# Performance work log

Measured on AMD Instinct MI355X. Metric: run time of the kernel, lower is better.

The kernel has to match this reference:

```python
import jax, jax.numpy as jnp
import numpy as np

NL, NS, NE = 16, 256, 100   # nlatent, nspatial, n_embd
B, P, T = 2, 2, 12


def _xavier(key, shape):
    # torch xavier_uniform: fan_in = shape[1]*prod(rest), fan_out = shape[0]*prod(rest)
    rf = int(np.prod(shape[2:])) if len(shape) > 2 else 1
    fan_in, fan_out = shape[1] * rf, shape[0] * rf
    b = float(np.sqrt(6.0 / (fan_in + fan_out)))
    return jax.random.uniform(key, shape, jnp.float32, -b, b)


def setup_inputs() -> dict:
    key = jax.random.key(0)
    ks = jax.random.split(key, 8)
    x = jax.random.normal(ks[0], (B, P, T, NL, NS), jnp.float32)
    K = _xavier(ks[1], (NS, NS, NL))
    Q = _xavier(ks[2], (NS, NS, NL))
    V = _xavier(ks[3], (NS, NS, NL))
    Aoo = jnp.ones((NS, NS), jnp.float32)
    # Ann is initialized to zeros in the module; use nonzero values so the
    # clamped geometric recurrence over time is actually exercised.
    Ann = jax.random.uniform(ks[4], (NE,), jnp.float32, -0.9, 0.9)
    Aon = _xavier(ks[5], (NS, NS, NE))
    Ano = _xavier(ks[6], (NS, NS, NE))
    w = jnp.ones((NS,), jnp.float32) / NS
    return {"x": x, "K": K, "Q": Q, "V": V, "Aoo": Aoo,
            "Ann": Ann, "Aon": Aon, "Ano": Ano, "w": w}


def reference(x, K, Q, V, Aoo, Ann, Aon, Ano, w):
    # kvt[B,p,T,X,Y] = sum_{x,c} Q[Y,x,c] K[X,x,c] x[B,p,T,c,x]
    kvt = jnp.einsum('Yxc,Xxc,BpTcx->BpTXY', Q, K, x)
    Aon_c = jnp.clip(Aon, -1.0, 1.0)
    Ano_c = jnp.clip(Ano, -1.0, 1.0)

    # t = T-1 term (elementwise Aoo) and t = T-2 term
    h = Aoo[None, None, None] * kvt[:, :, -1:]
    h = h + jnp.einsum('xyn,XYn,BpTXY->BpTxy', Aon_c, Ano_c, kvt[:, :, -2:-1])

    nT = x.shape[2]
    # Ann sequence used in the loop: A_2 = Ann (raw), A_{j+1} = clip(A_j * Ann)
    def step(a, _):
        return jnp.clip(a * Ann, -1.0, 1.0), a
    _, A_seq = jax.lax.scan(step, Ann, None, length=nT - 2)  # [T-2, n], A_seq[j-2]=A_j

    # loop index j=2..T-1 touches time slice t = T-1-j, i.e. t = T-3 .. 0
    s = jnp.einsum('XYn,BpJXY->BpJn', Ano_c, kvt[:, :, :nT - 2])  # J = t in 0..T-3
    A_t = A_seq[::-1]                       # align A_j with time index t = T-1-j
    s2 = jnp.einsum('Jn,BpJn->Bpn', A_t, s)
    h = h + jnp.einsum('xyn,Bpn->Bpxy', Aon_c, s2)[:, :, None]  # [B,p,1,x,y]

    q = jnp.einsum('Xxc,Bpcx->BpcX', V, x[:, :, -1])
    y = jnp.einsum('x,BpcX,BpTXx->BpTc', w, q, h)  # [B,p,1,c]
    return y
```

## Files before the change

kernel.cpp:

```cpp
#include <hip/hip_runtime.h>
#include <hip/hip_fp16.h>


using f32x4 = __attribute__((ext_vector_type(4))) float;
using half8 = __attribute__((ext_vector_type(8))) _Float16;
using half4 = __attribute__((ext_vector_type(4))) _Float16;

#define KVT_STRIDE 3145728ull
#define KS 4

__device__ inline float clip1(float v) { return fminf(fmaxf(v, -1.f), 1.f); }

__device__ inline half8 mul8(uint4 a, uint4 b) {
    half8 x = __builtin_bit_cast(half8, a);
    half8 y = __builtin_bit_cast(half8, b);
    return x * y;
}

__device__ __forceinline__ void gl_lds16(const void* g, void* l) {
    __builtin_amdgcn_global_load_lds(
        (const __attribute__((address_space(1))) void*)g,
        (__attribute__((address_space(3))) void*)l, 16, 0, 0);
}

__global__ void prep_kernel(const float* __restrict__ K, const float* __restrict__ Q,
                            const float* __restrict__ xin,
                            __half* __restrict__ Kh, __half* __restrict__ Qh,
                            __half* __restrict__ u_t)
{
    int b = blockIdx.x, t = threadIdx.x;
    if (b < 512) {
        bool isK = (b < 256);
        int bb = isK ? b : b - 256;
        size_t base = (size_t)bb * 4096 + t * 16;
        const f32x4* src = (const f32x4*)((isK ? K : Q) + base);
        __half* dst = (isK ? Kh : Qh) + base;
        #pragma unroll
        for (int j = 0; j < 2; ++j) {
            f32x4 v0 = src[j * 2], v1 = src[j * 2 + 1];
            half8 h;
            h[0] = (_Float16)v0.x; h[1] = (_Float16)v0.y;
            h[2] = (_Float16)v0.z; h[3] = (_Float16)v0.w;
            h[4] = (_Float16)v1.x; h[5] = (_Float16)v1.y;
            h[6] = (_Float16)v1.z; h[7] = (_Float16)v1.w;
            *(half8*)(dst + j * 8) = h;
        }
    } else {
        int bt = b - 512;
        const float* src = xin + (size_t)bt * 4096;
        int xx = t;
        half8 lo, hi;
        #pragma unroll
        for (int c = 0; c < 8; ++c)  lo[c] = (_Float16)src[c * 256 + xx];
        #pragma unroll
        for (int c = 0; c < 8; ++c)  hi[c] = (_Float16)src[(c + 8) * 256 + xx];
        half8* dst = (half8*)(u_t + (size_t)bt * 4096 + xx * 16);
        dst[0] = lo; dst[1] = hi;
    }
}

__global__ __launch_bounds__(256, 3) void gemm_kvt(
    const __half* __restrict__ Kh, const __half* __restrict__ Qh,
    const __half* __restrict__ u_t, __half* __restrict__ kvtp)
{
    __shared__ __half As[128][64];
    __shared__ __half Bs[2][128][64];
    __shared__ __half u_s[1024];

    int bid = blockIdx.x;
    int work = (bid & 7) * 96 + (bid >> 3);
    int kc = work / 192;
    int rem = work - kc * 192;
    int tile = rem / 48;
    int bt = rem - tile * 48;
    int Xb = (tile >> 1) * 128, Yb = (tile & 1) * 128;
    int kbase = kc * 1024;

    int tid = threadIdx.x;
    if (tid < 128)
        *(uint4*)&u_s[tid * 8] = *(const uint4*)(u_t + (size_t)bt * 4096 + kbase + tid * 8);
    __syncthreads();

    int wave = tid >> 6, lane = tid & 63;

    int arow = tid >> 1;
    int ap0 = (tid & 1) * 4;
    const __half* gA = Kh + (size_t)(Xb + arow) * 4096 + kbase + ap0 * 8;
    int arsw = arow & 7;

    int brow = wave * 32 + (lane >> 3);
    int bq = (lane & 7) ^ ((lane >> 3) & 7);
    const __half* gB = Qh + (size_t)(Yb + brow) * 4096 + kbase + bq * 8;

    int wr = (wave >> 1) * 64, wc = (wave & 1) * 64;
    int lrow = lane & 15, kg = lane >> 4;
    int fb0 = ((0 * 4 + kg) ^ (lrow & 7)) << 4;
    int fb1 = ((1 * 4 + kg) ^ (lrow & 7)) << 4;

    f32x4 acc[4][4];
    f32x4 zero = {0.f, 0.f, 0.f, 0.f};
    #pragma unroll
    for (int m = 0; m < 4; ++m)
        #pragma unroll
        for (int n = 0; n < 4; ++n) acc[m][n] = zero;

    #define LOAD_A(s, rg)                                                      \
        do {                                                                   \
            const __half* a_ = gA + (s) * 64;                                  \
            _Pragma("unroll")                                                  \
            for (int j_ = 0; j_ < 4; ++j_)                                     \
                rg[j_] = *(const uint4*)(a_ + j_ * 8);                         \
        } while (0)

    #define ISSUE_B(s, buf)                                                    \
        do {                                                                   \
            _Pragma("unroll")                                                  \
            for (int i_ = 0; i_ < 4; ++i_)                                     \
                gl_lds16(gB + (size_t)(i_ * 8) * 4096 + (s) * 64,              \
                         &Bs[buf][wave * 32 + i_ * 8][0]);                     \
        } while (0)

    #define WRITE_A(s, rg)                                                     \
        do {                                                                   \
            _Pragma("unroll")                                                  \
            for (int j_ = 0; j_ < 4; ++j_) {                                   \
                int p_ = ap0 + j_;                                             \
                uint4 uv_ = *(const uint4*)&u_s[(s) * 64 + p_ * 8];            \
                *(half8*)((char*)&As[arow][0] + ((p_ ^ arsw) << 4)) =          \
                    mul8(rg[j_], uv_);                                         \
            }                                                                  \
        } while (0)

    #define COMPUTE(cur)                                                       \
        do {                                                                   \
            _Pragma("unroll")                                                  \
            for (int kh = 0; kh < 2; ++kh) {                                   \
                int fbk = kh ? fb1 : fb0;                                      \
                half8 af[4], bf[4];                                            \
                _Pragma("unroll")                                              \
                for (int m = 0; m < 4; ++m)                                    \
                    af[m] = *(const half8*)((const char*)&As[wr + m * 16 + lrow][0] + fbk); \
                _Pragma("unroll")                                              \
                for (int n = 0; n < 4; ++n)                                    \
                    bf[n] = *(const half8*)((const char*)&Bs[cur][wc + n * 16 + lrow][0] + fbk); \
                _Pragma("unroll")                                              \
                for (int m = 0; m < 4; ++m)                                    \
                    _Pragma("unroll")                                          \
                    for (int n = 0; n < 4; ++n)                                \
                        acc[m][n] = __builtin_amdgcn_mfma_f32_16x16x32_f16(af[m], bf[n], acc[m][n], 0, 0, 0); \
            }                                                                  \
        } while (0)

    #define STEP(s, cset, iset, cur)                                           \
        do {                                                                   \
            if ((s) < 15) asm volatile("s_waitcnt vmcnt(8) lgkmcnt(0)" ::: "memory"); \
            else          asm volatile("s_waitcnt vmcnt(0) lgkmcnt(0)" ::: "memory"); \
            __builtin_amdgcn_s_barrier();                                      \
            __builtin_amdgcn_sched_barrier(0);                                 \
            COMPUTE(cur);                                                      \
            asm volatile("s_waitcnt lgkmcnt(0)" ::: "memory");                 \
            __builtin_amdgcn_s_barrier();                                      \
            __builtin_amdgcn_sched_barrier(0);                                 \
            if ((s) + 2 < 16) {                                                \
                LOAD_A((s) + 2, iset);                                         \
                ISSUE_B((s) + 2, cur);                                         \
            }                                                                  \
            if ((s) + 1 < 16) WRITE_A((s) + 1, cset);                          \
        } while (0)

    uint4 aP[4], aC[4];
    LOAD_A(0, aP);
    ISSUE_B(0, 0);
    LOAD_A(1, aC);
    ISSUE_B(1, 1);
    WRITE_A(0, aP);

    #pragma unroll
    for (int s = 0; s < 16; s += 2) {
        STEP(s,     aC, aP, 0);
        STEP(s + 1, aP, aC, 1);
    }
    #undef STEP
    #undef COMPUTE
    #undef WRITE_A
    #undef ISSUE_B
    #undef LOAD_A

    __half* outp = kvtp + (size_t)kc * KVT_STRIDE + (size_t)bt * 65536;
    int row0 = Xb + wr + kg * 4;
    int col0 = Yb + wc + lrow;
    #pragma unroll
    for (int m = 0; m < 4; ++m)
        #pragma unroll
        for (int n = 0; n < 4; ++n)
            #pragma unroll
            for (int rr = 0; rr < 4; ++rr)
                outp[(size_t)(row0 + m * 16 + rr) * 256 + col0 + n * 16] =
                    __float2half(acc[m][n][rr]);
}

__global__ __launch_bounds__(256) void mid_kernel(
    const float* __restrict__ Ano, const __half* __restrict__ kvtp,
    const float* __restrict__ V, const float* __restrict__ xin,
    const float* __restrict__ Aon, const float* __restrict__ wv,
    float* __restrict__ Sp, float* __restrict__ R, float* __restrict__ W2p)
{
    __shared__ __align__(16) char smem[49792];
    int b = blockIdx.x, tid = threadIdx.x;

    if (b < 256) {
        __half* anoA = (__half*)smem;
        __half* anoB = (__half*)(smem + 12928);
        float (*kvtA)[68] = (float(*)[68])(smem + 25856);
        float (*kvtB)[68] = (float(*)[68])(smem + 37824);
        int k0 = b * 256;

        int lane = tid & 63;
        int bp = tid >> 6;
        bool has2 = lane < 36;
        float acc0[11], acc1[11];
        #pragma unroll
        for (int J = 0; J < 11; ++J) { acc0[J] = 0.f; acc1[J] = 0.f; }

        f32x4 ar[7];
        half8 kr[2][4];

        #define LOAD_SP(cc)                                                    \
            do {                                                               \
                int k0s = k0 + (cc) * 64;                                      \
                const f32x4* asrc = (const f32x4*)(Ano + (size_t)k0s * 100);   \
                _Pragma("unroll")                                              \
                for (int it = 0; it < 7; ++it) {                               \
                    int i = tid + it * 256;                                    \
                    if (i < 1600) ar[it] = __builtin_nontemporal_load(asrc + i); \
                }                                                              \
                _Pragma("unroll")                                              \
                for (int it = 0; it < 2; ++it) {                               \
                    int idx = tid + it * 256;                                  \
                    if (idx < 352) {                                           \
                        int rI = idx >> 3, g = idx & 7;                        \
                        int bpr = rI / 11, Jr = rI - bpr * 11;                 \
                        const __half* p = kvtp + (size_t)(bpr * 12 + Jr) * 65536 + k0s + g * 8; \
                        kr[it][0] = *(const half8*)(p);                        \
                        kr[it][1] = *(const half8*)(p + KVT_STRIDE);           \
                        kr[it][2] = *(const half8*)(p + 2 * KVT_STRIDE);       \
                        kr[it][3] = *(const half8*)(p + 3 * KVT_STRIDE);       \
                    }                                                          \
                }                                                              \
            } while (0)

        #define WRITE_SP(anoDst, kvtDst)                                       \
            do {                                                               \
                _Pragma("unroll")                                              \
                for (int it = 0; it < 7; ++it) {                               \
                    int i = tid + it * 256;                                    \
                    if (i < 1600) {                                            \
                        half4 h;                                               \
                        h[0] = (_Float16)clip1(ar[it].x);                      \
                        h[1] = (_Float16)clip1(ar[it].y);                      \
                        h[2] = (_Float16)clip1(ar[it].z);                      \
                        h[3] = (_Float16)clip1(ar[it].w);                      \
                        *(half4*)&anoDst[i * 4] = h;                           \
                    }                                                          \
                }                                                              \
                _Pragma("unroll")                                              \
                for (int it = 0; it < 2; ++it) {                               \
                    int idx = tid + it * 256;                                  \
                    if (idx < 352) {                                           \
                        int rI = idx >> 3, g = idx & 7;                        \
                        f32x4 lo, hi;                                          \
                        _Pragma("unroll")                                      \
                        for (int j = 0; j < 4; ++j) {                          \
                            lo[j] = (float)kr[it][0][j] + (float)kr[it][1][j]  \
                                  + (float)kr[it][2][j] + (float)kr[it][3][j]; \
                            hi[j] = (float)kr[it][0][j+4] + (float)kr[it][1][j+4] \
                                  + (float)kr[it][2][j+4] + (float)kr[it][3][j+4]; \
                        }                                                      \
                        *(f32x4*)&kvtDst[rI][g * 8]     = lo;                  \
                        *(f32x4*)&kvtDst[rI][g * 8 + 4] = hi;                  \
                    }                                                          \
                }                                                              \
            } while (0)

        #define COMPUTE_SP(anoSrc, kvtSrc)                                     \
            do {                                                               \
                for (int k = 0; k < 64; k += 4) {                              \
                    f32x4 kv[11];                                              \
                    _Pragma("unroll")                                          \
                    for (int J = 0; J < 11; ++J)                               \
                        kv[J] = *(const f32x4*)&kvtSrc[bp * 11 + J][k];        \
                    _Pragma("unroll")                                          \
                    for (int kk = 0; kk < 4; ++kk) {                           \
                        float a0 = (float)anoSrc[(k + kk) * 100 + lane];       \
                        float a1r = (float)anoSrc[(k + kk) * 100 + 64 + lane]; \
                        float a1 = has2 ? a1r : 0.f;                           \
                        _Pragma("unroll")                                      \
                        for (int J = 0; J < 11; ++J) {                         \
                            acc0[J] += kv[J][kk] * a0;                         \
                            acc1[J] += kv[J][kk] * a1;                         \
                        }                                                      \
                    }                                                          \
                }                                                              \
            } while (0)

        LOAD_SP(0);
        WRITE_SP(anoA, kvtA);
        __syncthreads();
        LOAD_SP(1);
        COMPUTE_SP(anoA, kvtA);
        WRITE_SP(anoB, kvtB);
        __syncthreads();
        LOAD_SP(2);
        COMPUTE_SP(anoB, kvtB);
        WRITE_SP(anoA, kvtA);
        __syncthreads();
        LOAD_SP(3);
        COMPUTE_SP(anoA, kvtA);
        WRITE_SP(anoB, kvtB);
        __syncthreads();
        COMPUTE_SP(anoB, kvtB);

        #undef LOAD_SP
        #undef WRITE_SP
        #undef COMPUTE_SP

        float* outb = Sp + ((size_t)b * 4 + bp) * 1100;
        #pragma unroll
        for (int J = 0; J < 11; ++J) {
            outb[J * 100 + lane] = acc0[J];
            if (has2) outb[J * 100 + 64 + lane] = acc1[J];
        }
    } else if (b < 512) {
        float* vrow = (float*)smem;
        int X = b - 256;
        {
            const float4* src = (const float4*)(V + (size_t)X * 4096);
            float4* dst = (float4*)vrow;
            for (int i = tid; i < 1024; i += 256) dst[i] = src[i];
        }
        __syncthreads();
        int bp = tid >> 6, c = (tid >> 2) & 15, g = tid & 3;
        const float* xl = xin + ((size_t)(bp * 12) + 11) * 4096 + c * 256;
        float p0 = 0.f, p1 = 0.f;
        #pragma unroll 2
        for (int x = g * 64; x < g * 64 + 64; x += 2) {
            p0 += xl[x]     * vrow[x * 16 + c];
            p1 += xl[x + 1] * vrow[(x + 1) * 16 + c];
        }
        float p = p0 + p1;
        p += __shfl_xor(p, 1);
        p += __shfl_xor(p, 2);
        if (g == 0) R[((size_t)bp * 256 + X) * 16 + c] = p;
    } else {
        int idx = b - 512;
        int X = idx >> 1, h = idx & 1;
        int g = h * 2 + (tid >> 7), n = tid & 127;
        if (n < 100) {
            const float* base = Aon + (size_t)X * 25600 + (size_t)g * 6400 + n;
            const float* wb = wv + g * 64;
            float a0 = 0.f, a1 = 0.f, a2 = 0.f, a3 = 0.f;
            for (int bb = 0; bb < 64; bb += 4) {
                float v0 = __builtin_nontemporal_load(base + (size_t)(bb + 0) * 100);
                float v1 = __builtin_nontemporal_load(base + (size_t)(bb + 1) * 100);
                float v2 = __builtin_nontemporal_load(base + (size_t)(bb + 2) * 100);
                float v3 = __builtin_nontemporal_load(base + (size_t)(bb + 3) * 100);
                a0 += wb[bb + 0] * clip1(v0);
                a1 += wb[bb + 1] * clip1(v1);
                a2 += wb[bb + 2] * clip1(v2);
                a3 += wb[bb + 3] * clip1(v3);
            }
            W2p[((size_t)g * 256 + X) * 100 + n] = (a0 + a1) + (a2 + a3);
        }
    }
}

__global__ void reduce_s(const float* __restrict__ Sp, float* __restrict__ Sq,
                         float* __restrict__ out)
{
    int bid = blockIdx.x;
    int t = threadIdx.x;
    if (bid == 0 && t < 64) out[t] = 0.f;
    int qq = bid & 7, idx = bid >> 3;
    int bp = idx / 11, J = idx - bp * 11;
    if (t >= 100) return;
    float a0 = 0.f, a1 = 0.f, a2 = 0.f, a3 = 0.f;
    int c0 = qq * 32;
    for (int c = c0; c < c0 + 32; c += 4) {
        a0 += Sp[((size_t)(c + 0) * 4 + bp) * 1100 + J * 100 + t];
        a1 += Sp[((size_t)(c + 1) * 4 + bp) * 1100 + J * 100 + t];
        a2 += Sp[((size_t)(c + 2) * 4 + bp) * 1100 + J * 100 + t];
        a3 += Sp[((size_t)(c + 3) * 4 + bp) * 1100 + J * 100 + t];
    }
    Sq[(size_t)(qq * 44 + idx) * 100 + t] = (a0 + a1) + (a2 + a3);
}

__global__ __launch_bounds__(256) void hw_kernel(const float* __restrict__ Aoo,
                                                 const float* __restrict__ wv,
                                                 const __half* __restrict__ kvtp,
                                                 const float* __restrict__ W2p,
                                                 const float* __restrict__ Sq,
                                                 const float* __restrict__ Ann,
                                                 const float* __restrict__ R,
                                                 float* __restrict__ out)
{
    __shared__ float yp[4][16];
    __shared__ float c2s[128];
    int bp = blockIdx.x >> 6, Xg = blockIdx.x & 63;
    int tid = threadIdx.x;

    if (tid < 128) {
        int n = tid;
        float r = 0.f;
        if (n < 100) {
            float S[11];
            #pragma unroll
            for (int J = 0; J < 11; ++J) {
                float s = 0.f;
                #pragma unroll
                for (int qq = 0; qq < 8; ++qq)
                    s += Sq[(size_t)(qq * 44 + bp * 11 + J) * 100 + n];
                S[J] = s;
            }
            float a = Ann[n];
            float seq[10];
            float v = a;
            seq[0] = v;
            #pragma unroll
            for (int s2 = 1; s2 < 10; ++s2) { v = clip1(v * a); seq[s2] = v; }
            r = S[10];
            #pragma unroll
            for (int J = 0; J < 10; ++J)
                r += seq[9 - J] * S[J];
        }
        c2s[n] = r;
    }
    __syncthreads();

    int wave = tid >> 6, lane = tid & 63;
    int X = Xg * 4 + wave;
    size_t base = (size_t)(bp * 12 + 11) * 65536 + (size_t)X * 256;
    const float* ao = Aoo + (size_t)X * 256;
    float red = 0.f;
    #pragma unroll
    for (int qq = 0; qq < 4; ++qq) {
        int xx = qq * 64 + lane;
        float kvv = 0.f;
        #pragma unroll
        for (int c = 0; c < KS; ++c)
            kvv += __half2float(kvtp[(size_t)c * KVT_STRIDE + base + xx]);
        red += wv[xx] * ao[xx] * kvv;
    }
    float w2a = 0.f, w2b = 0.f;
    #pragma unroll
    for (int g = 0; g < 4; ++g) {
        w2a += W2p[((size_t)g * 256 + X) * 100 + lane];
        if (lane < 36) w2b += W2p[((size_t)g * 256 + X) * 100 + 64 + lane];
    }
    red += c2s[lane] * w2a;
    if (lane < 36)
        red += c2s[64 + lane] * w2b;
    #pragma unroll
    for (int off = 32; off; off >>= 1) red += __shfl_xor(red, off);
    if (lane < 16) yp[wave][lane] = red * R[((size_t)bp * 256 + X) * 16 + lane];
    __syncthreads();
    if (tid < 16) {
        float s = yp[0][tid] + yp[1][tid] + yp[2][tid] + yp[3][tid];
        atomicAdd(&out[bp * 16 + tid], s);
    }
}

extern "C" void kernel_launch(void* const* d_in, const int* in_sizes, int n_in,
                              void* d_out, int out_size, void* d_ws, size_t ws_size,
                              hipStream_t stream)
{
    const float* x   = (const float*)d_in[0];
    const float* K   = (const float*)d_in[1];
    const float* Q   = (const float*)d_in[2];
    const float* V   = (const float*)d_in[3];
    const float* Aoo = (const float*)d_in[4];
    const float* Ann = (const float*)d_in[5];
    const float* Aon = (const float*)d_in[6];
    const float* Ano = (const float*)d_in[7];
    const float* wv  = (const float*)d_in[8];
    float* out = (float*)d_out;

    char* ws = (char*)d_ws;
    const size_t o_Qh   = 0;
    const size_t o_Kh   = o_Qh + (size_t)2 * 1024 * 1024;
    const size_t o_ut   = o_Kh + (size_t)2 * 1024 * 1024;
    const size_t o_kvtp = o_ut + (size_t)512 * 1024;
    const size_t o_Sp   = o_kvtp + (size_t)KS * KVT_STRIDE * 2;
    const size_t o_Sq   = o_Sp + (size_t)256 * 4400 * 4;
    const size_t o_W2   = o_Sq + (size_t)35200 * 4 + 64;
    const size_t o_R    = o_W2 + (size_t)102400 * 4;

    __half* Qh  = (__half*)(ws + o_Qh);
    __half* Kh  = (__half*)(ws + o_Kh);
    __half* u_t = (__half*)(ws + o_ut);
    __half* kvtp = (__half*)(ws + o_kvtp);
    float* Sp   = (float*)(ws + o_Sp);
    float* Sq   = (float*)(ws + o_Sq);
    float* W2p  = (float*)(ws + o_W2);
    float* R    = (float*)(ws + o_R);

    hipLaunchKernelGGL(prep_kernel, dim3(560),  dim3(256), 0, stream,
                       K, Q, x, Kh, Qh, u_t);
    hipLaunchKernelGGL(gemm_kvt,    dim3(768),  dim3(256), 0, stream,
                       Kh, Qh, u_t, kvtp);
    hipLaunchKernelGGL(mid_kernel,  dim3(1024), dim3(256), 0, stream,
                       Ano, kvtp, V, x, Aon, wv, Sp, R, W2p);
    hipLaunchKernelGGL(reduce_s,    dim3(352),  dim3(128), 0, stream, Sp, Sq, out);
    hipLaunchKernelGGL(hw_kernel,   dim3(256),  dim3(256), 0, stream,
                       Aoo, wv, kvtp, W2p, Sq, Ann, R, out);
}
```

Before: 88.09 us.

## Replace reduce_s kernel with atomic accumulation in mid_kernel; vectorize hw loads

Each mid_kernel block now adds its partial S sums straight into the eight-way Sq buffer with float atomics, instead of writing per-block partials that a separate reduce_s kernel summed. Sq and out are zeroed by extra blocks added to prep_kernel. This removes one kernel launch and the round trip of the partial buffer through memory. In exchange it adds atomic contention (32 blocks per address) and a float summation order that varies from run to run. hw_kernel also switches to half4 and float4 vector loads for the kvt, w and Aoo reads.

```diff
diff --git a/kernel.cpp b/kernel.cpp
--- a/kernel.cpp
+++ b/kernel.cpp
@@ -26,7 +26,8 @@
 __global__ void prep_kernel(const float* __restrict__ K, const float* __restrict__ Q,
                             const float* __restrict__ xin,
                             __half* __restrict__ Kh, __half* __restrict__ Qh,
-                            __half* __restrict__ u_t)
+                            __half* __restrict__ u_t,
+                            float* __restrict__ Sq, float* __restrict__ out)
 {
     int b = blockIdx.x, t = threadIdx.x;
     if (b < 512) {
@@ -45,7 +46,7 @@
             h[6] = (_Float16)v1.z; h[7] = (_Float16)v1.w;
             *(half8*)(dst + j * 8) = h;
         }
-    } else {
+    } else if (b < 560) {
         int bt = b - 512;
         const float* src = xin + (size_t)bt * 4096;
         int xx = t;
@@ -56,6 +57,13 @@
         for (int c = 0; c < 8; ++c)  hi[c] = (_Float16)src[(c + 8) * 256 + xx];
         half8* dst = (half8*)(u_t + (size_t)bt * 4096 + xx * 16);
         dst[0] = lo; dst[1] = hi;
+    } else {
+        int zb = b - 560;
+        int i = zb * 1024 + t * 4;
+        f32x4 z = {0.f, 0.f, 0.f, 0.f};
+        if (i + 3 < 35200) *(f32x4*)(Sq + i) = z;
+        else for (int j = 0; j < 4; ++j) if (i + j < 35200) Sq[i + j] = 0.f;
+        if (zb == 0 && t < 64) out[t] = 0.f;
     }
 }
 
@@ -203,7 +211,7 @@
     const float* __restrict__ Ano, const __half* __restrict__ kvtp,
     const float* __restrict__ V, const float* __restrict__ xin,
     const float* __restrict__ Aon, const float* __restrict__ wv,
-    float* __restrict__ Sp, float* __restrict__ R, float* __restrict__ W2p)
+    float* __restrict__ Sq, float* __restrict__ R, float* __restrict__ W2p)
 {
     __shared__ __align__(16) char smem[49792];
     int b = blockIdx.x, tid = threadIdx.x;
@@ -324,11 +332,12 @@
         #undef WRITE_SP
         #undef COMPUTE_SP
 
-        float* outb = Sp + ((size_t)b * 4 + bp) * 1100;
+        int qq = b >> 5;
+        float* sqb = Sq + (size_t)(qq * 44 + bp * 11) * 100;
         #pragma unroll
         for (int J = 0; J < 11; ++J) {
-            outb[J * 100 + lane] = acc0[J];
-            if (has2) outb[J * 100 + 64 + lane] = acc1[J];
+            atomicAdd(&sqb[J * 100 + lane], acc0[J]);
+            if (has2) atomicAdd(&sqb[J * 100 + 64 + lane], acc1[J]);
         }
     } else if (b < 512) {
         float* vrow = (float*)smem;
@@ -374,26 +383,6 @@
     }
 }
 
-__global__ void reduce_s(const float* __restrict__ Sp, float* __restrict__ Sq,
-                         float* __restrict__ out)
-{
-    int bid = blockIdx.x;
-    int t = threadIdx.x;
-    if (bid == 0 && t < 64) out[t] = 0.f;
-    int qq = bid & 7, idx = bid >> 3;
-    int bp = idx / 11, J = idx - bp * 11;
-    if (t >= 100) return;
-    float a0 = 0.f, a1 = 0.f, a2 = 0.f, a3 = 0.f;
-    int c0 = qq * 32;
-    for (int c = c0; c < c0 + 32; c += 4) {
-        a0 += Sp[((size_t)(c + 0) * 4 + bp) * 1100 + J * 100 + t];
-        a1 += Sp[((size_t)(c + 1) * 4 + bp) * 1100 + J * 100 + t];
-        a2 += Sp[((size_t)(c + 2) * 4 + bp) * 1100 + J * 100 + t];
-        a3 += Sp[((size_t)(c + 3) * 4 + bp) * 1100 + J * 100 + t];
-    }
-    Sq[(size_t)(qq * 44 + idx) * 100 + t] = (a0 + a1) + (a2 + a3);
-}
-
 __global__ __launch_bounds__(256) void hw_kernel(const float* __restrict__ Aoo,
                                                  const float* __restrict__ wv,
                                                  const __half* __restrict__ kvtp,
@@ -438,17 +427,20 @@
 
     int wave = tid >> 6, lane = tid & 63;
     int X = Xg * 4 + wave;
-    size_t base = (size_t)(bp * 12 + 11) * 65536 + (size_t)X * 256;
-    const float* ao = Aoo + (size_t)X * 256;
+    size_t base = (size_t)(bp * 12 + 11) * 65536 + (size_t)X * 256 + lane * 4;
     float red = 0.f;
-    #pragma unroll
-    for (int qq = 0; qq < 4; ++qq) {
-        int xx = qq * 64 + lane;
-        float kvv = 0.f;
-        #pragma unroll
-        for (int c = 0; c < KS; ++c)
-            kvv += __half2float(kvtp[(size_t)c * KVT_STRIDE + base + xx]);
-        red += wv[xx] * ao[xx] * kvv;
+    {
+        f32x4 kvs = {0.f, 0.f, 0.f, 0.f};
+        #pragma unroll
+        for (int c = 0; c < KS; ++c) {
+            half4 v = *(const half4*)(kvtp + (size_t)c * KVT_STRIDE + base);
+            #pragma unroll
+            for (int i = 0; i < 4; ++i) kvs[i] += (float)v[i];
+        }
+        f32x4 w4  = *(const f32x4*)(wv + lane * 4);
+        f32x4 ao4 = *(const f32x4*)(Aoo + (size_t)X * 256 + lane * 4);
+        #pragma unroll
+        for (int i = 0; i < 4; ++i) red += w4[i] * ao4[i] * kvs[i];
     }
     float w2a = 0.f, w2b = 0.f;
     #pragma unroll
@@ -489,8 +481,7 @@
     const size_t o_Kh   = o_Qh + (size_t)2 * 1024 * 1024;
     const size_t o_ut   = o_Kh + (size_t)2 * 1024 * 1024;
     const size_t o_kvtp = o_ut + (size_t)512 * 1024;
-    const size_t o_Sp   = o_kvtp + (size_t)KS * KVT_STRIDE * 2;
-    const size_t o_Sq   = o_Sp + (size_t)256 * 4400 * 4;
+    const size_t o_Sq   = o_kvtp + (size_t)KS * KVT_STRIDE * 2;
     const size_t o_W2   = o_Sq + (size_t)35200 * 4 + 64;
     const size_t o_R    = o_W2 + (size_t)102400 * 4;
 
@@ -498,18 +489,16 @@
     __half* Kh  = (__half*)(ws + o_Kh);
     __half* u_t = (__half*)(ws + o_ut);
     __half* kvtp = (__half*)(ws + o_kvtp);
-    float* Sp   = (float*)(ws + o_Sp);
     float* Sq   = (float*)(ws + o_Sq);
     float* W2p  = (float*)(ws + o_W2);
     float* R    = (float*)(ws + o_R);
 
-    hipLaunchKernelGGL(prep_kernel, dim3(560),  dim3(256), 0, stream,
-                       K, Q, x, Kh, Qh, u_t);
+    hipLaunchKernelGGL(prep_kernel, dim3(595),  dim3(256), 0, stream,
+                       K, Q, x, Kh, Qh, u_t, Sq, out);
     hipLaunchKernelGGL(gemm_kvt,    dim3(768),  dim3(256), 0, stream,
                        Kh, Qh, u_t, kvtp);
     hipLaunchKernelGGL(mid_kernel,  dim3(1024), dim3(256), 0, stream,
-                       Ano, kvtp, V, x, Aon, wv, Sp, R, W2p);
-    hipLaunchKernelGGL(reduce_s,    dim3(352),  dim3(128), 0, stream, Sp, Sq, out);
+                       Ano, kvtp, V, x, Aon, wv, Sq, R, W2p);
     hipLaunchKernelGGL(hw_kernel,   dim3(256),  dim3(256), 0, stream,
                        Aoo, wv, kvtp, W2p, Sq, Ann, R, out);
 }
```

Result: no change. 87.99 us (-0.1%).
